# Kernel tuning notes

Hardware: AMD Instinct MI355X
Metric: run time of the kernel (lower is better)

Reference implementation:

```python
import jax, jax.numpy as jnp
import numpy as np

V, D, H, L, F, B, S = 512, 512, 8, 6, 2048, 8, 1024
DK = D // H
EPS = 1e-5


def _positional_encoding(max_len, d_model):
    pos = np.arange(max_len, dtype=np.float32)[:, None]
    div = np.exp(np.arange(0, d_model, 2, dtype=np.float32) * (-np.log(10000.0) / d_model))
    pe = np.zeros((max_len, d_model), dtype=np.float32)
    pe[:, 0::2] = np.sin(pos * div)
    pe[:, 1::2] = np.cos(pos * div)
    return jnp.asarray(pe)


def setup_inputs() -> dict:
    key = jax.random.key(0)
    ks = jax.random.split(key, 24)
    xavier = lambda k, shp: jax.random.normal(k, shp, jnp.float32) * np.sqrt(2.0 / (shp[-2] + shp[-1]))
    inp = {
        "input_ids": jax.random.randint(ks[0], (B, S), 0, V),
        "emb": jax.random.normal(ks[1], (V, D), jnp.float32) * 0.02,
        "pe": _positional_encoding(1024, D),
        "Wq": xavier(ks[2], (L, D, D)), "bq": jnp.zeros((L, D)),
        "Wk": xavier(ks[3], (L, D, D)), "bk": jnp.zeros((L, D)),
        "Wv": xavier(ks[4], (L, D, D)), "bv": jnp.zeros((L, D)),
        "Wo": xavier(ks[5], (L, D, D)), "bo": jnp.zeros((L, D)),
        "ln1_g": jnp.ones((L, D)), "ln1_b": jnp.zeros((L, D)),
        "W1": xavier(ks[6], (L, D, F)), "b1": jnp.zeros((L, F)),
        "W2": xavier(ks[7], (L, F, D)), "b2": jnp.zeros((L, D)),
        "ln2_g": jnp.ones((L, D)), "ln2_b": jnp.zeros((L, D)),
        "Wout": xavier(ks[8], (D, V)), "bout": jnp.zeros((V,)),
    }
    return inp


def _ln(x, g, b):
    mu = jnp.mean(x, -1, keepdims=True)
    var = jnp.mean(jnp.square(x - mu), -1, keepdims=True)
    return (x - mu) * jax.lax.rsqrt(var + EPS) * g + b


def reference(input_ids, emb, pe, Wq, bq, Wk, bk, Wv, bv, Wo, bo,
              ln1_g, ln1_b, W1, b1, W2, b2, ln2_g, ln2_b, Wout, bout):
    h = emb[input_ids] * np.sqrt(D) + pe[:S]  # [B,S,D]
    # Faithful to the original mask bug: masked_fill(mask==0, -1e9) fills the
    # LOWER triangle (incl diagonal); raw scores are kept strictly where j > i.
    r = jnp.arange(S)
    keep = r[None, :] > r[:, None]  # [S,S]

    def block(h, p):
        (wq, bq_, wk, bk_, wv, bv_, wo, bo_,
         g1, be1, w1, b1_, w2, b2_, g2, be2) = p
        split = lambda t: t.reshape(B, S, H, DK).transpose(0, 2, 1, 3)
        q = split(h @ wq + bq_)
        k = split(h @ wk + bk_)
        v = split(h @ wv + bv_)
        scores = jnp.einsum('bhqd,bhkd->bhqk', q, k) / np.sqrt(DK)
        scores = jnp.where(keep, scores, -1e9)
        a = jax.nn.softmax(scores, axis=-1)
        o = jnp.einsum('bhqk,bhkd->bhqd', a, v).transpose(0, 2, 1, 3).reshape(B, S, D)
        h = _ln(h + (o @ wo + bo_), g1, be1)
        f = jax.nn.relu(h @ w1 + b1_) @ w2 + b2_
        h = _ln(h + f, g2, be2)
        return h, None

    params = (Wq, bq, Wk, bk, Wv, bv, Wo, bo, ln1_g, ln1_b, W1, b1, W2, b2, ln2_g, ln2_b)
    h, _ = jax.lax.scan(block, h, params)
    return h @ Wout + bout  # logits [B,S,V]
```

## Files before the change

### kernel.cpp

```cpp
#include <hip/hip_runtime.h>

typedef unsigned short u16;
typedef __attribute__((ext_vector_type(8))) short bf16x8;
typedef __attribute__((ext_vector_type(4))) float f32x4;
typedef __attribute__((ext_vector_type(4))) unsigned int uint4v;
typedef __attribute__((ext_vector_type(4))) unsigned short us4;

#define NLAYER 6
#define D_MODEL 512
#define NHEAD 8
#define DKH 64
#define SEQ 1024
#define BATCH 8
#define FFN 2048
#define MROWS (BATCH * SEQ)
#define QKV_LD 1536
#define SCALE_LOG2E 0.18033688011112042f

__device__ __forceinline__ float b2f(u16 u) {
  union { unsigned u32; float f; } x; x.u32 = ((unsigned)u) << 16; return x.f;
}
__device__ __forceinline__ u16 f2b(float f) {
  union { float f; unsigned u; } x; x.f = f;
  unsigned r = x.u + 0x7FFFu + ((x.u >> 16) & 1u);
  return (u16)(r >> 16);
}
__device__ __forceinline__ void gld16(const u16* g, u16* l) {
  __builtin_amdgcn_global_load_lds(
      (const __attribute__((address_space(1))) unsigned int*)g,
      (__attribute__((address_space(3))) unsigned int*)l, 16, 0, 0);
}
__device__ __forceinline__ void barrier_raw() {
  asm volatile("" ::: "memory");
  __builtin_amdgcn_s_barrier();
  asm volatile("" ::: "memory");
}

__global__ __launch_bounds__(256) void transpose_cvt_kernel(
    const float* __restrict__ src, u16* __restrict__ dst, int K, int N, size_t dstZ,
    float scale)
{
  __shared__ float t[32][33];
  const int z = blockIdx.z;
  src += (size_t)z * K * N;
  dst += (size_t)z * dstZ;
  const int n0 = blockIdx.x * 32, k0 = blockIdx.y * 32;
  const int tx = threadIdx.x, ty = threadIdx.y;
#pragma unroll
  for (int i = 0; i < 32; i += 8)
    t[ty + i][tx] = src[(size_t)(k0 + ty + i) * N + n0 + tx];
  __syncthreads();
#pragma unroll
  for (int i = 0; i < 32; i += 8)
    dst[(size_t)(n0 + ty + i) * K + k0 + tx] = f2b(t[tx][ty + i] * scale);
}

__global__ __launch_bounds__(256) void concat_bias_kernel(
    const float* __restrict__ bq, const float* __restrict__ bk,
    const float* __restrict__ bv, float* __restrict__ dst)
{
  const int l = blockIdx.x, t = threadIdx.x;
#pragma unroll
  for (int j = t; j < 512; j += 256) {
    dst[l * QKV_LD + j]        = bq[l * 512 + j] * SCALE_LOG2E;
    dst[l * QKV_LD + 512 + j]  = bk[l * 512 + j];
    dst[l * QKV_LD + 1024 + j] = bv[l * 512 + j];
  }
}

__global__ __launch_bounds__(256) void embed_kernel(
    const int* __restrict__ ids, const float* __restrict__ emb,
    const float* __restrict__ pe, float* __restrict__ Hf, u16* __restrict__ Hb)
{
  const int row = blockIdx.x;
  const int s = row & (SEQ - 1);
  const int id = ids[row];
  const int tid = threadIdx.x;
#pragma unroll
  for (int u = 0; u < 2; ++u) {
    const int d = tid + u * 256;
    float v = emb[(size_t)id * D_MODEL + d] * 22.62741699796952f + pe[(size_t)s * D_MODEL + d];
    Hf[(size_t)row * D_MODEL + d] = v;
    Hb[(size_t)row * D_MODEL + d] = f2b(v);
  }
}

template<int BMT, bool RELU, bool OUTF, bool OUTB, bool VT>
__global__ __launch_bounds__(256) void gemm_kernel(
    const u16* __restrict__ A, const u16* __restrict__ Bt,
    const float* __restrict__ bias,
    float* __restrict__ Cf, u16* __restrict__ Cb, u16* __restrict__ Vtp,
    int M, int N, int K)
{
  constexpr int IT = BMT / 32;
  constexpr int AHALF = BMT * 64;
  constexpr int BHALF = 128 * 64;
  __shared__ __align__(16) u16 As[2 * AHALF];
  __shared__ __align__(16) u16 Bs[2 * BHALF];
  const int tid = threadIdx.x;
  const int bm = blockIdx.x * BMT, bn = blockIdx.y * 128;
  const int wave = tid >> 6, lane = tid & 63;
  const int lm = lane & 15, quad = lane >> 4;
  const int wm = (wave & 1) * (BMT / 2), wn = (wave >> 1) * 64;

  const int sr = tid >> 3;
  const int sc = (tid & 7) ^ (sr & 7);
  const u16* Ap = A  + (size_t)(bm + sr) * K + sc * 8;
  const u16* Bp = Bt + (size_t)(bn + sr) * K + sc * 8;
  u16* lA = As + wave * 512;
  u16* lB = Bs + wave * 512;

  f32x4 acc[IT][4] = {};

  const int nt = K >> 6;
  auto stage = [&](int buf, int t) {
    const size_t ko = (size_t)t << 6;
#pragma unroll
    for (int p = 0; p < BMT / 32; ++p)
      gld16(Ap + (size_t)(p * 32) * K + ko, lA + buf * AHALF + p * 2048);
#pragma unroll
    for (int p = 0; p < 4; ++p)
      gld16(Bp + (size_t)(p * 32) * K + ko, lB + buf * BHALF + p * 2048);
  };

  stage(0, 0);
  __syncthreads();

  for (int t = 0; t < nt; ++t) {
    const int cur = t & 1;
    if (t + 1 < nt) stage(cur ^ 1, t + 1);
    const u16* as = As + cur * AHALF;
    const u16* bs = Bs + cur * BHALF;
#pragma unroll
    for (int kh = 0; kh < 2; ++kh) {
      bf16x8 af[IT], bg[4];
#pragma unroll
      for (int i = 0; i < IT; ++i) {
        const int row = wm + i * 16 + lm;
        af[i] = *(const bf16x8*)&as[row * 64 + (((kh * 4 + quad) ^ (row & 7)) << 3)];
      }
#pragma unroll
      for (int j = 0; j < 4; ++j) {
        const int row = wn + j * 16 + lm;
        bg[j] = *(const bf16x8*)&bs[row * 64 + (((kh * 4 + quad) ^ (row & 7)) << 3)];
      }
#pragma unroll
      for (int i = 0; i < IT; ++i)
#pragma unroll
        for (int j = 0; j < 4; ++j)
          acc[i][j] = __builtin_amdgcn_mfma_f32_16x16x32_bf16(af[i], bg[j], acc[i][j], 0, 0, 0);
    }
    __syncthreads();
  }

  const int mbase = bm + wm + quad * 4;
  const int nbase = bn + wn + lm;
#pragma unroll
  for (int i = 0; i < IT; ++i) {
#pragma unroll
    for (int j = 0; j < 4; ++j) {
      const int n = nbase + j * 16;
      const float bv = bias[n];
      float vv[4];
#pragma unroll
      for (int r = 0; r < 4; ++r) {
        float v = acc[i][j][r] + bv;
        if (RELU) v = fmaxf(v, 0.f);
        vv[r] = v;
      }
      if (VT && n >= 1024) {
        const int hh = (n - 1024) >> 6, d = (n - 1024) & 63;
        const int mm = mbase + i * 16;
        const int bb = mm >> 10, ss = mm & 1023;
        us4 pk;
#pragma unroll
        for (int r = 0; r < 4; ++r) pk[r] = f2b(vv[r]);
        *(us4*)&Vtp[(((size_t)(bb * NHEAD + hh)) * 64 + d) * SEQ + ss] = pk;
      } else {
#pragma unroll
        for (int r = 0; r < 4; ++r) {
          const int m = mbase + i * 16 + r;
          if (OUTF) Cf[(size_t)m * N + n] = vv[r];
          if (OUTB) Cb[(size_t)m * N + n] = f2b(vv[r]);
        }
      }
    }
  }
}

template<bool RELU, bool VT>
__global__ __launch_bounds__(512, 2) void gemm256_kernel(
    const u16* __restrict__ A, const u16* __restrict__ Bt,
    const float* __restrict__ bias,
    u16* __restrict__ Cb, u16* __restrict__ Vtp,
    int M, int N, int K)
{
  extern __shared__ __align__(16) u16 smem[];
  u16* ringA = smem;
  u16* ringB = smem + 32768;
  const int tid = threadIdx.x;
  const int wave = tid >> 6, lane = tid & 63;
  const int lm = lane & 15, quad = lane >> 4;
  const int wm = wave >> 2, wn = wave & 3;
  const int bm = blockIdx.x * 256, bn = blockIdx.y * 256;

  const u16* srcA[2];
  const u16* srcB[2];
  u16* dstA[2];
  u16* dstB[2];
#pragma unroll
  for (int g = 0; g < 2; ++g) {
    const int u = wave * 128 + g * 64 + lane;
    const int line = u >> 3, cph = u & 7;
    const int clog = cph ^ (line & 7);
    const int r = 2 * line + (clog >> 2);
    const int kq = clog & 3;
    srcA[g] = A  + (size_t)(bm + r) * K + kq * 8;
    srcB[g] = Bt + (size_t)(bn + r) * K + kq * 8;
    dstA[g] = ringA + wave * 1024 + g * 512;
    dstB[g] = ringB + wave * 1024 + g * 512;
  }

  const int NT = K >> 5;
  auto stage = [&](int buf, int t) {
    const size_t ko = (size_t)t << 5;
#pragma unroll
    for (int g = 0; g < 2; ++g) gld16(srcA[g] + ko, dstA[g] + buf * 8192);
#pragma unroll
    for (int g = 0; g < 2; ++g) gld16(srcB[g] + ko, dstB[g] + buf * 8192);
  };

  f32x4 acc[8][4] = {};

  stage(0, 0);
  stage(1, 1);

  const int cs = ((quad + ((lm & 1) << 2)) ^ ((lm >> 1) & 7)) << 3;
  const int aoff = (wm * 64 + (lm >> 1)) * 64 + cs;
  const int boff = (wn * 32 + (lm >> 1)) * 64 + cs;

#pragma unroll 1
  for (int t = 0; t < NT; ++t) {
    if (t + 1 < NT) asm volatile("s_waitcnt vmcnt(4)" ::: "memory");
    else            asm volatile("s_waitcnt vmcnt(0)" ::: "memory");
    barrier_raw();
    if (t + 2 < NT) stage((t + 2) & 3, t + 2);
    const u16* as_ = ringA + (t & 3) * 8192 + aoff;
    const u16* bs_ = ringB + (t & 3) * 8192 + boff;
    bf16x8 af[8], bg[4];
#pragma unroll
    for (int i = 0; i < 8; ++i) af[i] = *(const bf16x8*)&as_[i * 512];
#pragma unroll
    for (int j = 0; j < 4; ++j) bg[j] = *(const bf16x8*)&bs_[j * 512];
    __builtin_amdgcn_s_setprio(1);
#pragma unroll
    for (int i = 0; i < 8; ++i)
#pragma unroll
      for (int j = 0; j < 4; ++j)
        acc[i][j] = __builtin_amdgcn_mfma_f32_16x16x32_bf16(af[i], bg[j], acc[i][j], 0, 0, 0);
    __builtin_amdgcn_s_setprio(0);
  }

  const int mbase = bm + wm * 128 + quad * 4;
  const int nbase = bn + wn * 64 + lm;
#pragma unroll
  for (int i = 0; i < 8; ++i) {
#pragma unroll
    for (int j = 0; j < 4; ++j) {
      const int n = nbase + j * 16;
      const float bv = bias[n];
      float vv[4];
#pragma unroll
      for (int r = 0; r < 4; ++r) {
        float v = acc[i][j][r] + bv;
        if (RELU) v = fmaxf(v, 0.f);
        vv[r] = v;
      }
      if (VT && n >= 1024) {
        const int hh = (n - 1024) >> 6, d = (n - 1024) & 63;
        const int mm = mbase + i * 16;
        const int bb = mm >> 10, ss = mm & 1023;
        us4 pk;
#pragma unroll
        for (int r = 0; r < 4; ++r) pk[r] = f2b(vv[r]);
        *(us4*)&Vtp[(((size_t)(bb * NHEAD + hh)) * 64 + d) * SEQ + ss] = pk;
      } else {
#pragma unroll
        for (int r = 0; r < 4; ++r) {
          const int m = mbase + i * 16 + r;
          Cb[(size_t)m * N + n] = f2b(vv[r]);
        }
      }
    }
  }
}

template<bool LN>
__global__ __launch_bounds__(512, 2) void gemm_ln_kernel(
    const u16* __restrict__ A, const u16* __restrict__ Bt,
    const float* __restrict__ bias,
    const float* __restrict__ gw, const float* __restrict__ bw,
    float* __restrict__ Hf, u16* __restrict__ Hb, float* __restrict__ Cf,
    int K)
{
  extern __shared__ __align__(16) u16 smem[];
  u16* Asm = smem;
  u16* Bsm = smem + 4096;
  float* red = (float*)(smem + 69632);
  const int tid = threadIdx.x;
  const int wave = tid >> 6, lane = tid & 63;
  const int lm = lane & 15, quad = lane >> 4, l7 = lm & 7;
  const int bm = blockIdx.x * 32;

  const int srow = tid >> 3;
  const int scg = (tid & 7) ^ (srow & 7);
  const u16* Ap = A  + (size_t)(bm + srow) * K + scg * 8;
  const u16* Bp = Bt + (size_t)srow * K + scg * 8;
  u16* uA = Asm + wave * 512;
  u16* uB = Bsm + wave * 512;

  f32x4 acc[2][4] = {};
  const int NT = K >> 6;
  auto stage = [&](int buf, int t) {
    const size_t ko = (size_t)t << 6;
    if (wave < 4) gld16(Ap + ko, uA + buf * 2048);
#pragma unroll
    for (int p = 0; p < 8; ++p)
      gld16(Bp + (size_t)(p * 64) * K + ko, uB + buf * 32768 + p * 4096);
  };

  stage(0, 0);
  __syncthreads();

#pragma unroll 1
  for (int t = 0; t < NT; ++t) {
    const int cur = t & 1;
    if (t + 1 < NT) stage(cur ^ 1, t + 1);
    const u16* as_ = Asm + cur * 2048 + lm * 64;
    const u16* bs_ = Bsm + cur * 32768 + (wave * 64 + lm) * 64;
#pragma unroll
    for (int kh = 0; kh < 2; ++kh) {
      const int slot = ((kh * 4 + quad) ^ l7) << 3;
      bf16x8 af[2], bg[4];
      af[0] = *(const bf16x8*)&as_[slot];
      af[1] = *(const bf16x8*)&as_[1024 + slot];
#pragma unroll
      for (int j = 0; j < 4; ++j)
        bg[j] = *(const bf16x8*)&bs_[j * 1024 + slot];
#pragma unroll
      for (int i = 0; i < 2; ++i)
#pragma unroll
        for (int j = 0; j < 4; ++j)
          acc[i][j] = __builtin_amdgcn_mfma_f32_16x16x32_bf16(af[i], bg[j], acc[i][j], 0, 0, 0);
    }
    __syncthreads();
  }

  const int col0 = wave * 64 + lm;
  float bi[4];
#pragma unroll
  for (int j = 0; j < 4; ++j) bi[j] = bias[col0 + j * 16];

  if (LN) {
    float gv[4], bv[4];
#pragma unroll
    for (int j = 0; j < 4; ++j) { gv[j] = gw[col0 + j * 16]; bv[j] = bw[col0 + j * 16]; }
    float x[2][4][4];
    float ps[8], pq[8];
#pragma unroll
    for (int k = 0; k < 8; ++k) { ps[k] = 0.f; pq[k] = 0.f; }
#pragma unroll
    for (int i = 0; i < 2; ++i)
#pragma unroll
      for (int r = 0; r < 4; ++r) {
        const int rowl = i * 16 + quad * 4 + r;
        const size_t rb = (size_t)(bm + rowl) * D_MODEL;
#pragma unroll
        for (int j = 0; j < 4; ++j) {
          float xv = acc[i][j][r] + bi[j] + Hf[rb + col0 + j * 16];
          x[i][j][r] = xv;
          ps[i * 4 + r] += xv;
          pq[i * 4 + r] += xv * xv;
        }
      }
#pragma unroll
    for (int o = 1; o < 16; o <<= 1)
#pragma unroll
      for (int k = 0; k < 8; ++k) {
        ps[k] += __shfl_xor(ps[k], o, 16);
        pq[k] += __shfl_xor(pq[k], o, 16);
      }
    if (lm == 0) {
#pragma unroll
      for (int k = 0; k < 8; ++k) {
        const int rowl = (k >> 2) * 16 + quad * 4 + (k & 3);
        red[wave * 32 + rowl] = ps[k];
        red[256 + wave * 32 + rowl] = pq[k];
      }
    }
    __syncthreads();
    if (tid < 32) {
      float s = 0.f, q = 0.f;
#pragma unroll
      for (int w = 0; w < 8; ++w) { s += red[w * 32 + tid]; q += red[256 + w * 32 + tid]; }
      const float mu = s * (1.f / 512.f);
      const float var = q * (1.f / 512.f) - mu * mu;
      red[512 + tid] = mu;
      red[544 + tid] = rsqrtf(var + 1e-5f);
    }
    __syncthreads();
#pragma unroll
    for (int i = 0; i < 2; ++i)
#pragma unroll
      for (int r = 0; r < 4; ++r) {
        const int rowl = i * 16 + quad * 4 + r;
        const float mu = red[512 + rowl];
        const float rs = red[544 + rowl];
        const size_t rb = (size_t)(bm + rowl) * D_MODEL;
#pragma unroll
        for (int j = 0; j < 4; ++j) {
          const float y = (x[i][j][r] - mu) * rs * gv[j] + bv[j];
          Hf[rb + col0 + j * 16] = y;
          Hb[rb + col0 + j * 16] = f2b(y);
        }
      }
  } else {
#pragma unroll
    for (int i = 0; i < 2; ++i)
#pragma unroll
      for (int r = 0; r < 4; ++r) {
        const int rowl = i * 16 + quad * 4 + r;
        const size_t rb = (size_t)(bm + rowl) * D_MODEL;
#pragma unroll
        for (int j = 0; j < 4; ++j)
          Cf[rb + col0 + j * 16] = acc[i][j][r] + bi[j];
      }
  }
}

__global__ __launch_bounds__(256) void attn_mfma_kernel(
    const u16* __restrict__ QKV, const u16* __restrict__ Vt, u16* __restrict__ O)
{
  __shared__ __align__(16) u16 Ks[64 * 64];
  __shared__ __align__(16) u16 Vs[64 * 64];
  __shared__ __align__(16) u16 Ps[4 * 16 * 64];
  const int tid = threadIdx.x;
  const int wave = tid >> 6, lane = tid & 63;
  const int quad = lane >> 4, l15 = lane & 15;
  const int l7 = l15 & 7;
  const int id = blockIdx.x;
  const int bh = id & 63;
  const int b = bh >> 3, h = bh & 7;
  const int g = id >> 6;
  const int u = g * 4 + wave;
  u16* psw = Ps + wave * (16 * 64);
  const size_t qoff = (size_t)b * SEQ * QKV_LD + h * 64;
  const size_t vtb  = (size_t)bh * 64 * SEQ;

  const int sr = tid >> 3, sc = tid & 7;
  const u16* kg0 = QKV + qoff + 512 + (size_t)sr * QKV_LD + sc * 8;
  const u16* kg1 = kg0 + (size_t)32 * QKV_LD;
  const u16* vg0 = Vt + vtb + (size_t)sr * SEQ + sc * 8;
  const u16* vg1 = vg0 + (size_t)32 * SEQ;
  const int sw = (sc ^ (sr & 7)) << 3;
  u16* ks0 = &Ks[sr * 64 + sw];
  u16* ks1 = &Ks[(sr + 32) * 64 + sw];
  u16* vs0 = &Vs[sr * 64 + sw];
  u16* vs1 = &Vs[(sr + 32) * 64 + sw];

  const u16* qp = QKV + qoff + (size_t)(u * 16 + l15) * QKV_LD + quad * 8;
  const bf16x8 qf0 = *(const bf16x8*)(qp);
  const bf16x8 qf1 = *(const bf16x8*)(qp + 32);

  f32x4 oacc[4] = {};
  float lsum[4] = {0.f, 0.f, 0.f, 0.f};

  uint4v kr0 = *(const uint4v*)(kg0 + (size_t)(g * 64) * QKV_LD);
  uint4v kr1 = *(const uint4v*)(kg1 + (size_t)(g * 64) * QKV_LD);
  uint4v vr0 = *(const uint4v*)(vg0 + g * 64);
  uint4v vr1 = *(const uint4v*)(vg1 + g * 64);

#pragma unroll 1
  for (int jt = g; jt < 16; ++jt) {
    __syncthreads();
    *(uint4v*)ks0 = kr0; *(uint4v*)ks1 = kr1;
    *(uint4v*)vs0 = vr0; *(uint4v*)vs1 = vr1;
    __syncthreads();
    if (jt < 15) {
      kr0 = *(const uint4v*)(kg0 + (size_t)((jt + 1) * 64) * QKV_LD);
      kr1 = *(const uint4v*)(kg1 + (size_t)((jt + 1) * 64) * QKV_LD);
      vr0 = *(const uint4v*)(vg0 + (jt + 1) * 64);
      vr1 = *(const uint4v*)(vg1 + (jt + 1) * 64);
    }
    f32x4 sacc[4] = {};
#pragma unroll
    for (int nt = 0; nt < 4; ++nt) {
      const int key = nt * 16 + l15, k7 = key & 7;
      bf16x8 kb0 = *(const bf16x8*)&Ks[key * 64 + ((quad ^ k7) << 3)];
      bf16x8 kb1 = *(const bf16x8*)&Ks[key * 64 + (((quad + 4) ^ k7) << 3)];
      sacc[nt] = __builtin_amdgcn_mfma_f32_16x16x32_bf16(qf0, kb0, sacc[nt], 0, 0, 0);
      sacc[nt] = __builtin_amdgcn_mfma_f32_16x16x32_bf16(qf1, kb1, sacc[nt], 0, 0, 0);
    }
    const bool diag = (jt == g);
#pragma unroll
    for (int nt = 0; nt < 4; ++nt)
#pragma unroll
      for (int r = 0; r < 4; ++r) {
        float pv = __builtin_amdgcn_exp2f(sacc[nt][r]);
        if (diag) {
          const int i = u * 16 + quad * 4 + r;
          const int j = jt * 64 + nt * 16 + l15;
          pv = (j > i) ? pv : 0.f;
        }
        lsum[r] += pv;
        const int qr = quad * 4 + r;
        const int j2 = nt * 16 + l15;
        psw[qr * 64 + (((j2 >> 3) ^ (qr & 7)) << 3) + (j2 & 7)] = f2b(pv);
      }
    bf16x8 pf0 = *(const bf16x8*)&psw[l15 * 64 + (((quad + 0) ^ l7) << 3)];
    bf16x8 pf1 = *(const bf16x8*)&psw[l15 * 64 + (((quad + 4) ^ l7) << 3)];
#pragma unroll
    for (int nt = 0; nt < 4; ++nt) {
      const int d = nt * 16 + l15, d7 = d & 7;
      bf16x8 vb0 = *(const bf16x8*)&Vs[d * 64 + ((quad ^ d7) << 3)];
      bf16x8 vb1 = *(const bf16x8*)&Vs[d * 64 + (((quad + 4) ^ d7) << 3)];
      oacc[nt] = __builtin_amdgcn_mfma_f32_16x16x32_bf16(pf0, vb0, oacc[nt], 0, 0, 0);
      oacc[nt] = __builtin_amdgcn_mfma_f32_16x16x32_bf16(pf1, vb1, oacc[nt], 0, 0, 0);
    }
  }

#pragma unroll
  for (int o = 1; o < 16; o <<= 1)
#pragma unroll
    for (int r = 0; r < 4; ++r) lsum[r] += __shfl_xor(lsum[r], o, 16);
  float rl[4];
#pragma unroll
  for (int r = 0; r < 4; ++r) rl[r] = 1.0f / lsum[r];
#pragma unroll
  for (int nt = 0; nt < 4; ++nt)
#pragma unroll
    for (int r = 0; r < 4; ++r) {
      const int row = u * 16 + quad * 4 + r;
      O[(size_t)(b * SEQ + row) * D_MODEL + h * DKH + nt * 16 + l15] = f2b(oacc[nt][r] * rl[r]);
    }

  if (g == 15) {
    __syncthreads();
    const int d = tid >> 2, scv = (tid & 3) * 256;
    const u16* pv = Vt + vtb + (size_t)d * SEQ + scv;
    float s = 0.f;
#pragma unroll 8
    for (int i2 = 0; i2 < 256; ++i2) s += b2f(pv[i2]);
    s += __shfl_xor(s, 1, 64);
    s += __shfl_xor(s, 2, 64);
    if ((tid & 3) == 0)
      O[((size_t)b * SEQ + SEQ - 1) * D_MODEL + h * 64 + d] = f2b(s * (1.f / SEQ));
  }
}

__global__ __launch_bounds__(256) void add_ln_kernel(
    const float* __restrict__ Hin, const u16* __restrict__ T,
    const float* __restrict__ g, const float* __restrict__ bta,
    float* __restrict__ Hout, u16* __restrict__ Hb)
{
  __shared__ float red[8];
  const int row = blockIdx.x, tid = threadIdx.x;
  const int wave = tid >> 6, lane = tid & 63;
  const size_t base = (size_t)row * D_MODEL;
  const float x0 = Hin[base + tid] + b2f(T[base + tid]);
  const float x1 = Hin[base + tid + 256] + b2f(T[base + tid + 256]);
  float s = x0 + x1;
#pragma unroll
  for (int o = 32; o > 0; o >>= 1) s += __shfl_xor(s, o, 64);
  if (lane == 0) red[wave] = s;
  __syncthreads();
  const float mu = (red[0] + red[1] + red[2] + red[3]) * (1.f / 512.f);
  const float d0 = x0 - mu, d1 = x1 - mu;
  float v = d0 * d0 + d1 * d1;
#pragma unroll
  for (int o = 32; o > 0; o >>= 1) v += __shfl_xor(v, o, 64);
  if (lane == 0) red[4 + wave] = v;
  __syncthreads();
  const float var = (red[4] + red[5] + red[6] + red[7]) * (1.f / 512.f);
  const float rs = rsqrtf(var + 1e-5f);
  const float y0 = d0 * rs * g[tid] + bta[tid];
  const float y1 = d1 * rs * g[tid + 256] + bta[tid + 256];
  Hout[base + tid] = y0;
  Hout[base + tid + 256] = y1;
  Hb[base + tid] = f2b(y0);
  Hb[base + tid + 256] = f2b(y1);
}

extern "C" void kernel_launch(void* const* d_in, const int* in_sizes, int n_in,
                              void* d_out, int out_size, void* d_ws, size_t ws_size,
                              hipStream_t stream) {
  (void)in_sizes; (void)n_in; (void)out_size; (void)ws_size;
  const int*   ids  = (const int*)  d_in[0];
  const float* emb  = (const float*)d_in[1];
  const float* pe   = (const float*)d_in[2];
  const float* Wq   = (const float*)d_in[3];
  const float* bq   = (const float*)d_in[4];
  const float* Wk   = (const float*)d_in[5];
  const float* bk   = (const float*)d_in[6];
  const float* Wv   = (const float*)d_in[7];
  const float* bv   = (const float*)d_in[8];
  const float* Wo   = (const float*)d_in[9];
  const float* bo   = (const float*)d_in[10];
  const float* g1   = (const float*)d_in[11];
  const float* be1  = (const float*)d_in[12];
  const float* W1   = (const float*)d_in[13];
  const float* b1   = (const float*)d_in[14];
  const float* W2   = (const float*)d_in[15];
  const float* b2   = (const float*)d_in[16];
  const float* g2   = (const float*)d_in[17];
  const float* be2  = (const float*)d_in[18];
  const float* Wout = (const float*)d_in[19];
  const float* bout = (const float*)d_in[20];
  float* out = (float*)d_out;

  static int attr_set = 0;
  if (!attr_set) {
    hipFuncSetAttribute(reinterpret_cast<const void*>(&gemm256_kernel<false, true>),
                        hipFuncAttributeMaxDynamicSharedMemorySize, 131072);
    hipFuncSetAttribute(reinterpret_cast<const void*>(&gemm256_kernel<true, false>),
                        hipFuncAttributeMaxDynamicSharedMemorySize, 131072);
    hipFuncSetAttribute(reinterpret_cast<const void*>(&gemm_ln_kernel<true>),
                        hipFuncAttributeMaxDynamicSharedMemorySize, 141568);
    hipFuncSetAttribute(reinterpret_cast<const void*>(&gemm_ln_kernel<false>),
                        hipFuncAttributeMaxDynamicSharedMemorySize, 141568);
    attr_set = 1;
  }

  char* wsp = (char*)d_ws;
  auto alloc = [&](size_t bytes) -> char* {
    char* p = wsp; wsp += (bytes + 255) & ~(size_t)255; return p;
  };
  const size_t dd  = (size_t)D_MODEL * D_MODEL;
  const size_t df  = (size_t)D_MODEL * FFN;
  const size_t dq  = (size_t)QKV_LD * D_MODEL;
  u16* wqkv_t = (u16*)alloc(NLAYER * dq * 2);
  u16* wo_t   = (u16*)alloc(NLAYER * dd * 2);
  u16* w1_t   = (u16*)alloc(NLAYER * df * 2);
  u16* w2_t   = (u16*)alloc(NLAYER * df * 2);
  u16* wout_t = (u16*)alloc(dd * 2);
  float* bqkv = (float*)alloc(NLAYER * QKV_LD * 4);
  float* hf   = (float*)alloc((size_t)MROWS * D_MODEL * 4);
  u16*   hb   = (u16*)  alloc((size_t)MROWS * D_MODEL * 2);
  u16*   qkvb = (u16*)  alloc((size_t)MROWS * QKV_LD * 2);
  u16*   ob   = (u16*)  alloc((size_t)MROWS * D_MODEL * 2);
  u16*   vt   = (u16*)  alloc((size_t)BATCH * NHEAD * DKH * SEQ * 2);
  u16*   tb   = (u16*)  alloc((size_t)MROWS * D_MODEL * 2);
  u16*   mid  = qkvb;

  dim3 tb8(32, 8);
  transpose_cvt_kernel<<<dim3(16, 16, NLAYER), tb8, 0, stream>>>(Wq, wqkv_t,            512, 512,  dq, SCALE_LOG2E);
  transpose_cvt_kernel<<<dim3(16, 16, NLAYER), tb8, 0, stream>>>(Wk, wqkv_t + 512*512,  512, 512,  dq, 1.f);
  transpose_cvt_kernel<<<dim3(16, 16, NLAYER), tb8, 0, stream>>>(Wv, wqkv_t + 1024*512, 512, 512,  dq, 1.f);
  transpose_cvt_kernel<<<dim3(16, 16, NLAYER), tb8, 0, stream>>>(Wo, wo_t,   512, 512,  dd, 1.f);
  transpose_cvt_kernel<<<dim3(64, 16, NLAYER), tb8, 0, stream>>>(W1, w1_t,   512, 2048, df, 1.f);
  transpose_cvt_kernel<<<dim3(16, 64, NLAYER), tb8, 0, stream>>>(W2, w2_t,   2048, 512, df, 1.f);
  transpose_cvt_kernel<<<dim3(16, 16, 1),      tb8, 0, stream>>>(Wout, wout_t, 512, 512, dd, 1.f);
  concat_bias_kernel<<<NLAYER, 256, 0, stream>>>(bq, bk, bv, bqkv);

  embed_kernel<<<MROWS, 256, 0, stream>>>(ids, emb, pe, hf, hb);

  for (int l = 0; l < NLAYER; ++l) {
    gemm256_kernel<false, true><<<dim3(32, 6), 512, 131072, stream>>>(
        hb, wqkv_t + l * dq, bqkv + l * QKV_LD, qkvb, vt, MROWS, QKV_LD, 512);
    attn_mfma_kernel<<<1024, 256, 0, stream>>>(qkvb, vt, ob);
    gemm_ln_kernel<true><<<256, 512, 141568, stream>>>(
        ob, wo_t + l * dd, bo + l * 512, g1 + l * 512, be1 + l * 512,
        hf, hb, nullptr, 512);
    gemm256_kernel<true, false><<<dim3(32, 8), 512, 131072, stream>>>(
        hb, w1_t + l * df, b1 + l * 2048, mid, nullptr, MROWS, 2048, 512);
    gemm_kernel<64, false, false, true, false><<<dim3(128, 4), 256, 0, stream>>>(
        mid, w2_t + l * df, b2 + l * 512, nullptr, tb, nullptr, MROWS, 512, 2048);
    add_ln_kernel<<<MROWS, 256, 0, stream>>>(hf, tb, g2 + l * 512, be2 + l * 512, hf, hb);
  }
  gemm_ln_kernel<false><<<256, 512, 141568, stream>>>(
      hb, wout_t, bout, nullptr, nullptr, nullptr, nullptr, out, 512);
}
```

Before: 967.4 us.

## Stage two key/value tiles per barrier in attention and merge weight-transpose launches

The attention kernel now loads K and V for two 64-key tiles (128 keys) into double LDS buffers per iteration, halving the number of sync-barrier pairs and issuing larger prefetches. Blocks whose starting tile is odd skip the first half via a continue. Separately, five square weight transpose/convert launches are merged into one kernel indexed by blockIdx.z, cutting launch overhead. The cost is more registers and LDS per block, plus some redundant loading of a skipped half tile.

```diff
diff --git a/kernel.cpp b/kernel.cpp
--- a/kernel.cpp
+++ b/kernel.cpp
@@ -36,6 +36,33 @@
   asm volatile("" ::: "memory");
 }
 
+__global__ __launch_bounds__(256) void transpose_cvt5_kernel(
+    const float* __restrict__ Wq, const float* __restrict__ Wk,
+    const float* __restrict__ Wv, const float* __restrict__ Wo,
+    const float* __restrict__ Wout,
+    u16* __restrict__ wqkv_t, u16* __restrict__ wo_t, u16* __restrict__ wout_t)
+{
+  __shared__ float t[32][33];
+  const int z = blockIdx.z;
+  const float* src;
+  u16* dst;
+  float scale = 1.f;
+  if (z < 6)       { src = Wq + (size_t)z * 262144;        dst = wqkv_t + (size_t)z * 786432;                   scale = SCALE_LOG2E; }
+  else if (z < 12) { src = Wk + (size_t)(z - 6) * 262144;  dst = wqkv_t + (size_t)(z - 6) * 786432 + 512 * 512; }
+  else if (z < 18) { src = Wv + (size_t)(z - 12) * 262144; dst = wqkv_t + (size_t)(z - 12) * 786432 + 1024 * 512; }
+  else if (z < 24) { src = Wo + (size_t)(z - 18) * 262144; dst = wo_t + (size_t)(z - 18) * 262144; }
+  else             { src = Wout;                           dst = wout_t; }
+  const int n0 = blockIdx.x * 32, k0 = blockIdx.y * 32;
+  const int tx = threadIdx.x, ty = threadIdx.y;
+#pragma unroll
+  for (int i = 0; i < 32; i += 8)
+    t[ty + i][tx] = src[(size_t)(k0 + ty + i) * 512 + n0 + tx];
+  __syncthreads();
+#pragma unroll
+  for (int i = 0; i < 32; i += 8)
+    dst[(size_t)(n0 + ty + i) * 512 + k0 + tx] = f2b(t[tx][ty + i] * scale);
+}
+
 __global__ __launch_bounds__(256) void transpose_cvt_kernel(
     const float* __restrict__ src, u16* __restrict__ dst, int K, int N, size_t dstZ,
     float scale)
@@ -441,8 +468,8 @@
 __global__ __launch_bounds__(256) void attn_mfma_kernel(
     const u16* __restrict__ QKV, const u16* __restrict__ Vt, u16* __restrict__ O)
 {
-  __shared__ __align__(16) u16 Ks[64 * 64];
-  __shared__ __align__(16) u16 Vs[64 * 64];
+  __shared__ __align__(16) u16 Ks[2][64 * 64];
+  __shared__ __align__(16) u16 Vs[2][64 * 64];
   __shared__ __align__(16) u16 Ps[4 * 16 * 64];
   const int tid = threadIdx.x;
   const int wave = tid >> 6, lane = tid & 63;
@@ -458,15 +485,9 @@
   const size_t vtb  = (size_t)bh * 64 * SEQ;
 
   const int sr = tid >> 3, sc = tid & 7;
-  const u16* kg0 = QKV + qoff + 512 + (size_t)sr * QKV_LD + sc * 8;
-  const u16* kg1 = kg0 + (size_t)32 * QKV_LD;
-  const u16* vg0 = Vt + vtb + (size_t)sr * SEQ + sc * 8;
-  const u16* vg1 = vg0 + (size_t)32 * SEQ;
+  const u16* kg = QKV + qoff + 512 + (size_t)sr * QKV_LD + sc * 8;
+  const u16* vg = Vt + vtb + (size_t)sr * SEQ + sc * 8;
   const int sw = (sc ^ (sr & 7)) << 3;
-  u16* ks0 = &Ks[sr * 64 + sw];
-  u16* ks1 = &Ks[(sr + 32) * 64 + sw];
-  u16* vs0 = &Vs[sr * 64 + sw];
-  u16* vs1 = &Vs[(sr + 32) * 64 + sw];
 
   const u16* qp = QKV + qoff + (size_t)(u * 16 + l15) * QKV_LD + quad * 8;
   const bf16x8 qf0 = *(const bf16x8*)(qp);
@@ -475,57 +496,74 @@
   f32x4 oacc[4] = {};
   float lsum[4] = {0.f, 0.f, 0.f, 0.f};
 
-  uint4v kr0 = *(const uint4v*)(kg0 + (size_t)(g * 64) * QKV_LD);
-  uint4v kr1 = *(const uint4v*)(kg1 + (size_t)(g * 64) * QKV_LD);
-  uint4v vr0 = *(const uint4v*)(vg0 + g * 64);
-  uint4v vr1 = *(const uint4v*)(vg1 + g * 64);
+  const int T0 = g >> 1;
+  uint4v kr[4], vr[4];
+  auto ldpair = [&](int T) {
+    const size_t kb = (size_t)T * 128;
+    kr[0] = *(const uint4v*)(kg + (kb +  0) * QKV_LD);
+    kr[1] = *(const uint4v*)(kg + (kb + 32) * QKV_LD);
+    kr[2] = *(const uint4v*)(kg + (kb + 64) * QKV_LD);
+    kr[3] = *(const uint4v*)(kg + (kb + 96) * QKV_LD);
+    vr[0] = *(const uint4v*)(vg + kb);
+    vr[1] = *(const uint4v*)(vg + (size_t)32 * SEQ + kb);
+    vr[2] = *(const uint4v*)(vg + kb + 64);
+    vr[3] = *(const uint4v*)(vg + (size_t)32 * SEQ + kb + 64);
+  };
+
+  ldpair(T0);
 
 #pragma unroll 1
-  for (int jt = g; jt < 16; ++jt) {
+  for (int T = T0; T < 8; ++T) {
     __syncthreads();
-    *(uint4v*)ks0 = kr0; *(uint4v*)ks1 = kr1;
-    *(uint4v*)vs0 = vr0; *(uint4v*)vs1 = vr1;
+    *(uint4v*)&Ks[0][sr * 64 + sw] = kr[0];
+    *(uint4v*)&Ks[0][(sr + 32) * 64 + sw] = kr[1];
+    *(uint4v*)&Ks[1][sr * 64 + sw] = kr[2];
+    *(uint4v*)&Ks[1][(sr + 32) * 64 + sw] = kr[3];
+    *(uint4v*)&Vs[0][sr * 64 + sw] = vr[0];
+    *(uint4v*)&Vs[0][(sr + 32) * 64 + sw] = vr[1];
+    *(uint4v*)&Vs[1][sr * 64 + sw] = vr[2];
+    *(uint4v*)&Vs[1][(sr + 32) * 64 + sw] = vr[3];
     __syncthreads();
-    if (jt < 15) {
-      kr0 = *(const uint4v*)(kg0 + (size_t)((jt + 1) * 64) * QKV_LD);
-      kr1 = *(const uint4v*)(kg1 + (size_t)((jt + 1) * 64) * QKV_LD);
-      vr0 = *(const uint4v*)(vg0 + (jt + 1) * 64);
-      vr1 = *(const uint4v*)(vg1 + (jt + 1) * 64);
-    }
-    f32x4 sacc[4] = {};
-#pragma unroll
-    for (int nt = 0; nt < 4; ++nt) {
-      const int key = nt * 16 + l15, k7 = key & 7;
-      bf16x8 kb0 = *(const bf16x8*)&Ks[key * 64 + ((quad ^ k7) << 3)];
-      bf16x8 kb1 = *(const bf16x8*)&Ks[key * 64 + (((quad + 4) ^ k7) << 3)];
-      sacc[nt] = __builtin_amdgcn_mfma_f32_16x16x32_bf16(qf0, kb0, sacc[nt], 0, 0, 0);
-      sacc[nt] = __builtin_amdgcn_mfma_f32_16x16x32_bf16(qf1, kb1, sacc[nt], 0, 0, 0);
-    }
-    const bool diag = (jt == g);
-#pragma unroll
-    for (int nt = 0; nt < 4; ++nt)
-#pragma unroll
-      for (int r = 0; r < 4; ++r) {
-        float pv = __builtin_amdgcn_exp2f(sacc[nt][r]);
-        if (diag) {
-          const int i = u * 16 + quad * 4 + r;
-          const int j = jt * 64 + nt * 16 + l15;
-          pv = (j > i) ? pv : 0.f;
+    if (T + 1 < 8) ldpair(T + 1);
+#pragma unroll
+    for (int half = 0; half < 2; ++half) {
+      const int jt64 = 2 * T + half;
+      if (jt64 < g) continue;
+      f32x4 sacc[4] = {};
+#pragma unroll
+      for (int nt = 0; nt < 4; ++nt) {
+        const int key = nt * 16 + l15, k7 = key & 7;
+        bf16x8 kb0 = *(const bf16x8*)&Ks[half][key * 64 + ((quad ^ k7) << 3)];
+        bf16x8 kb1 = *(const bf16x8*)&Ks[half][key * 64 + (((quad + 4) ^ k7) << 3)];
+        sacc[nt] = __builtin_amdgcn_mfma_f32_16x16x32_bf16(qf0, kb0, sacc[nt], 0, 0, 0);
+        sacc[nt] = __builtin_amdgcn_mfma_f32_16x16x32_bf16(qf1, kb1, sacc[nt], 0, 0, 0);
+      }
+      const bool diag = (jt64 == g);
+#pragma unroll
+      for (int nt = 0; nt < 4; ++nt)
+#pragma unroll
+        for (int r = 0; r < 4; ++r) {
+          float pv = __builtin_amdgcn_exp2f(sacc[nt][r]);
+          if (diag) {
+            const int i = u * 16 + quad * 4 + r;
+            const int j = jt64 * 64 + nt * 16 + l15;
+            pv = (j > i) ? pv : 0.f;
+          }
+          lsum[r] += pv;
+          const int qr = quad * 4 + r;
+          const int j2 = nt * 16 + l15;
+          psw[qr * 64 + (((j2 >> 3) ^ (qr & 7)) << 3) + (j2 & 7)] = f2b(pv);
         }
-        lsum[r] += pv;
-        const int qr = quad * 4 + r;
-        const int j2 = nt * 16 + l15;
-        psw[qr * 64 + (((j2 >> 3) ^ (qr & 7)) << 3) + (j2 & 7)] = f2b(pv);
-      }
-    bf16x8 pf0 = *(const bf16x8*)&psw[l15 * 64 + (((quad + 0) ^ l7) << 3)];
-    bf16x8 pf1 = *(const bf16x8*)&psw[l15 * 64 + (((quad + 4) ^ l7) << 3)];
-#pragma unroll
-    for (int nt = 0; nt < 4; ++nt) {
-      const int d = nt * 16 + l15, d7 = d & 7;
-      bf16x8 vb0 = *(const bf16x8*)&Vs[d * 64 + ((quad ^ d7) << 3)];
-      bf16x8 vb1 = *(const bf16x8*)&Vs[d * 64 + (((quad + 4) ^ d7) << 3)];
-      oacc[nt] = __builtin_amdgcn_mfma_f32_16x16x32_bf16(pf0, vb0, oacc[nt], 0, 0, 0);
-      oacc[nt] = __builtin_amdgcn_mfma_f32_16x16x32_bf16(pf1, vb1, oacc[nt], 0, 0, 0);
+      bf16x8 pf0 = *(const bf16x8*)&psw[l15 * 64 + (((quad + 0) ^ l7) << 3)];
+      bf16x8 pf1 = *(const bf16x8*)&psw[l15 * 64 + (((quad + 4) ^ l7) << 3)];
+#pragma unroll
+      for (int nt = 0; nt < 4; ++nt) {
+        const int d = nt * 16 + l15, d7 = d & 7;
+        bf16x8 vb0 = *(const bf16x8*)&Vs[half][d * 64 + ((quad ^ d7) << 3)];
+        bf16x8 vb1 = *(const bf16x8*)&Vs[half][d * 64 + (((quad + 4) ^ d7) << 3)];
+        oacc[nt] = __builtin_amdgcn_mfma_f32_16x16x32_bf16(pf0, vb0, oacc[nt], 0, 0, 0);
+        oacc[nt] = __builtin_amdgcn_mfma_f32_16x16x32_bf16(pf1, vb1, oacc[nt], 0, 0, 0);
+      }
     }
   }
 
@@ -653,13 +691,10 @@
   u16*   mid  = qkvb;
 
   dim3 tb8(32, 8);
-  transpose_cvt_kernel<<<dim3(16, 16, NLAYER), tb8, 0, stream>>>(Wq, wqkv_t,            512, 512,  dq, SCALE_LOG2E);
-  transpose_cvt_kernel<<<dim3(16, 16, NLAYER), tb8, 0, stream>>>(Wk, wqkv_t + 512*512,  512, 512,  dq, 1.f);
-  transpose_cvt_kernel<<<dim3(16, 16, NLAYER), tb8, 0, stream>>>(Wv, wqkv_t + 1024*512, 512, 512,  dq, 1.f);
-  transpose_cvt_kernel<<<dim3(16, 16, NLAYER), tb8, 0, stream>>>(Wo, wo_t,   512, 512,  dd, 1.f);
+  transpose_cvt5_kernel<<<dim3(16, 16, 25), tb8, 0, stream>>>(
+      Wq, Wk, Wv, Wo, Wout, wqkv_t, wo_t, wout_t);
   transpose_cvt_kernel<<<dim3(64, 16, NLAYER), tb8, 0, stream>>>(W1, w1_t,   512, 2048, df, 1.f);
   transpose_cvt_kernel<<<dim3(16, 64, NLAYER), tb8, 0, stream>>>(W2, w2_t,   2048, 512, df, 1.f);
-  transpose_cvt_kernel<<<dim3(16, 16, 1),      tb8, 0, stream>>>(Wout, wout_t, 512, 512, dd, 1.f);
   concat_bias_kernel<<<NLAYER, 256, 0, stream>>>(bq, bk, bv, bqkv);
 
   embed_kernel<<<MROWS, 256, 0, stream>>>(ids, emb, pe, hf, hb);
```

Result: slower. 990.6 us (+2.4%).
